# Kernel tuning notes

Hardware: AMD Instinct MI355X
Metric: run time of the kernel (lower is better)

## Reference

```python
import jax, jax.numpy as jnp
import numpy as np

B, S, H, HEADS = 4, 2048, 512, 8
DK = H // HEADS
LN_EPS = 1e-5
NEG_INF = -1e30


def setup_inputs() -> dict:
    key = jax.random.key(0)
    k = jax.random.split(key, 6)
    x = jax.random.normal(k[0], (B, S, H), dtype=jnp.float32)
    mask = jax.random.randint(k[1], (B, S), 0, 2, dtype=jnp.int32)
    # per-head Q/K/V projection weights stacked: [heads, H, dk]
    Wq = jax.random.normal(k[2], (HEADS, H, DK), dtype=jnp.float32) * 0.05
    Wk = jax.random.normal(k[3], (HEADS, H, DK), dtype=jnp.float32) * 0.05
    Wv = jax.random.normal(k[4], (HEADS, H, DK), dtype=jnp.float32) * 0.05
    # output projection: [heads*dk, H] (y = h @ Wo)
    Wo = jax.random.normal(k[5], (HEADS * DK, H), dtype=jnp.float32) * 0.05
    gamma = jnp.ones((H,), dtype=jnp.float32)
    beta = jnp.zeros((H,), dtype=jnp.float32)
    return {"x": x, "mask": mask, "Wq": Wq, "Wk": Wk, "Wv": Wv,
            "Wo": Wo, "gamma": gamma, "beta": beta}


def reference(x, mask, Wq, Wk, Wv, Wo, gamma, beta):
    # LayerNorm over hidden dim
    mu = jnp.mean(x, axis=-1, keepdims=True)
    var = jnp.mean(jnp.square(x - mu), axis=-1, keepdims=True)
    xn = (x - mu) * jax.lax.rsqrt(var + LN_EPS) * gamma + beta  # [B,S,H]

    mf = mask.astype(jnp.float32)  # [B,S]

    # batched per-head projections (original loops over heads)
    q = jnp.einsum('bsh,nhd->bnsd', xn, Wq)  # [B,heads,S,dk]
    kk = jnp.einsum('bsh,nhd->bnsd', xn, Wk)
    v = jnp.einsum('bsh,nhd->bnsd', xn, Wv)

    scores = jnp.einsum('bnqd,bnkd->bnqk', q, kk) / np.sqrt(DK).astype(np.float32)
    m = mf[:, None, None, :]  # [B,1,1,S] broadcast over query dim
    logits = m * scores + (1.0 - m) * NEG_INF
    probs = jax.nn.softmax(logits, axis=-1)
    attn = jnp.einsum('bnqk,bnkd->bnqd', probs, v)  # [B,heads,S,dk]

    h = attn.transpose(0, 2, 1, 3).reshape(x.shape[0], x.shape[1], HEADS * DK)
    out = h @ Wo + xn          # residual adds post-norm x (as in original)
    out = out * mf[:, :, None]  # zero out masked positions
    return out
```

## Files before the change

kernel.cpp:

```cpp
#include <hip/hip_runtime.h>
#include <hip/hip_bf16.h>
#include <math.h>

#define B_ 4
#define S_ 2048
#define H_ 512
#define HEADS_ 8
#define DK_ 64
#define NROWS_ (B_*S_)
#define LN_EPS_ 1e-5f
#define NEG_INF_ -1e30f
#define QSCALE_ (0.125f * 1.44269504088896f)

typedef short s8v __attribute__((ext_vector_type(8)));
typedef short s4v __attribute__((ext_vector_type(4)));
typedef float f4v __attribute__((ext_vector_type(4)));

typedef __attribute__((address_space(1))) unsigned int gu32_t;
typedef __attribute__((address_space(3))) unsigned int lu32_t;

__device__ __forceinline__ unsigned short f2bf(float f) {
    unsigned int u = __float_as_uint(f);
    u += 0x7FFFu + ((u >> 16) & 1u);
    return (unsigned short)(u >> 16);
}

__device__ __forceinline__ float bf2f(unsigned short u) {
    return __uint_as_float((unsigned int)u << 16);
}

__device__ __forceinline__ s4v pk4bf(float a, float b, float c, float d) {
    union { __hip_bfloat162 h[2]; s4v v; } u;
    u.h[0] = __float22bfloat162_rn(float2{a, b});
    u.h[1] = __float22bfloat162_rn(float2{c, d});
    return u.v;
}

__global__ __launch_bounds__(256) void prep_kernel(
        const float* __restrict__ x, const float* __restrict__ gamma,
        const float* __restrict__ beta, const int* __restrict__ mask,
        const float* __restrict__ Wq, const float* __restrict__ Wk,
        const float* __restrict__ Wv, const float* __restrict__ Wo,
        unsigned short* __restrict__ xnb, float* __restrict__ mb,
        unsigned short* __restrict__ Wt) {
    int bx = blockIdx.x;
    if (bx < 2048) {
        int row  = bx * 4 + (threadIdx.x >> 6);
        int lane = threadIdx.x & 63;
        const float4* xr = (const float4*)(x + (size_t)row * H_ + lane * 8);
        float4 a = xr[0], d = xr[1];
        float s  = (a.x + a.y) + (a.z + a.w) + (d.x + d.y) + (d.z + d.w);
        float ss = (a.x*a.x + a.y*a.y) + (a.z*a.z + a.w*a.w)
                 + (d.x*d.x + d.y*d.y) + (d.z*d.z + d.w*d.w);
        #pragma unroll
        for (int i = 1; i < 64; i <<= 1) {
            s  += __shfl_xor(s, i, 64);
            ss += __shfl_xor(ss, i, 64);
        }
        float mu  = s * (1.f / 512.f);
        float var = ss * (1.f / 512.f) - mu * mu;
        float rstd = rsqrtf(var + LN_EPS_);
        if (lane == 0) mb[row] = mask[row] ? 0.f : NEG_INF_;
        const float4* gp = (const float4*)(gamma + lane * 8);
        const float4* bp = (const float4*)(beta + lane * 8);
        float4 g0 = gp[0], g1 = gp[1], b0 = bp[0], b1 = bp[1];
        float4 y0, y1;
        y0.x = (a.x - mu) * rstd * g0.x + b0.x;
        y0.y = (a.y - mu) * rstd * g0.y + b0.y;
        y0.z = (a.z - mu) * rstd * g0.z + b0.z;
        y0.w = (a.w - mu) * rstd * g0.w + b0.w;
        y1.x = (d.x - mu) * rstd * g1.x + b1.x;
        y1.y = (d.y - mu) * rstd * g1.y + b1.y;
        y1.z = (d.z - mu) * rstd * g1.z + b1.z;
        y1.w = (d.w - mu) * rstd * g1.w + b1.w;
        union { s4v h[2]; s8v v; } pk;
        pk.h[0] = pk4bf(y0.x, y0.y, y0.z, y0.w);
        pk.h[1] = pk4bf(y1.x, y1.y, y1.z, y1.w);
        *(s8v*)(xnb + (size_t)row * H_ + lane * 8) = pk.v;
    } else {
        __shared__ float tile[32][33];
        int wid = bx - 2048;
        const float* src;
        int ld, drow, k0, c0;
        float scale = 1.f;
        if (wid < 768) {
            int z = wid >> 5, rem = wid & 31;
            int cx = rem & 1, ky = rem >> 1;
            k0 = ky * 32; c0 = cx * 32;
            int zw = z >> 3, head = z & 7;
            const float* W = (zw == 0) ? Wq : (zw == 1) ? Wk : Wv;
            if (zw == 0) scale = QSCALE_;
            src = W + (size_t)head * H_ * DK_;
            ld = DK_;
            drow = zw * 512 + head * 64;
        } else {
            int rem = wid - 768;
            int cx = rem & 15, ky = rem >> 4;
            k0 = ky * 32; c0 = cx * 32;
            src = Wo; ld = H_; drow = 1536;
        }
        int tx = threadIdx.x & 31, ty = threadIdx.x >> 5;
        #pragma unroll
        for (int i = 0; i < 4; i++)
            tile[ty * 4 + i][tx] = src[(size_t)(k0 + ty * 4 + i) * ld + c0 + tx];
        __syncthreads();
        #pragma unroll
        for (int i = 0; i < 4; i++) {
            int cc = ty * 4 + i;
            Wt[(size_t)(drow + c0 + cc) * 512 + k0 + tx] = f2bf(tile[tx][cc] * scale);
        }
    }
}

__device__ __forceinline__ void gemm_tile(
        const unsigned short* __restrict__ A,
        const unsigned short* __restrict__ Bt,
        int r0, int j0, f4v acc[4][4]) {
    __shared__ unsigned short As[2 * 128 * 32];
    __shared__ unsigned short Bs[2 * 128 * 32];
    int t = threadIdx.x;
    int wv = t >> 6, L = t & 63, c = L & 15, g = L >> 4;
    int m_base = (wv & 1) * 64, n_base = (wv >> 1) * 64;
    #pragma unroll
    for (int i = 0; i < 4; i++)
        #pragma unroll
        for (int j = 0; j < 4; j++) acc[i][j] = (f4v){0.f, 0.f, 0.f, 0.f};
    for (int k0 = 0; k0 < 512; k0 += 64) {
        __syncthreads();
        #pragma unroll
        for (int half = 0; half < 2; half++) {
            #pragma unroll
            for (int i = 0; i < 2; i++) {
                int u = wv * 128 + i * 64 + L;
                int row = u >> 2, k16 = u & 3;
                __builtin_amdgcn_global_load_lds(
                    (const gu32_t*)(A + (size_t)(r0 + row) * 512 + k0 + half * 32 + k16 * 8),
                    (lu32_t*)(As + half * 4096 + (size_t)(wv * 128 + i * 64) * 8), 16, 0, 0);
                __builtin_amdgcn_global_load_lds(
                    (const gu32_t*)(Bt + (size_t)(j0 + row) * 512 + k0 + half * 32 + k16 * 8),
                    (lu32_t*)(Bs + half * 4096 + (size_t)(wv * 128 + i * 64) * 8), 16, 0, 0);
            }
        }
        __asm__ volatile("s_waitcnt vmcnt(0)" ::: "memory");
        __syncthreads();
        #pragma unroll
        for (int half = 0; half < 2; half++) {
            s8v a[4], b[4];
            #pragma unroll
            for (int i = 0; i < 4; i++)
                a[i] = *(const s8v*)(As + half * 4096 + (size_t)(m_base + i * 16 + c) * 32 + g * 8);
            #pragma unroll
            for (int j = 0; j < 4; j++)
                b[j] = *(const s8v*)(Bs + half * 4096 + (size_t)(n_base + j * 16 + c) * 32 + g * 8);
            #pragma unroll
            for (int i = 0; i < 4; i++)
                #pragma unroll
                for (int j = 0; j < 4; j++)
                    acc[i][j] = __builtin_amdgcn_mfma_f32_16x16x32_bf16(
                        a[i], b[j], acc[i][j], 0, 0, 0);
        }
    }
}

__global__ __launch_bounds__(256) void qkv_gemm(
        const unsigned short* __restrict__ xnb,
        const unsigned short* __restrict__ Wt,
        unsigned short* __restrict__ Qb, unsigned short* __restrict__ Kf,
        unsigned short* __restrict__ Vf) {
    f4v acc[4][4];
    int t = threadIdx.x;
    int wv = t >> 6, L = t & 63, c = L & 15, g = L >> 4;
    int rb = wv & 1, cb = wv >> 1;
    if (blockIdx.x < 8) {
        int m0 = blockIdx.x * 128, n0 = blockIdx.y * 128;
        gemm_tile(Wt, xnb, m0, n0, acc);
        int R0 = m0 + rb * 64;
        int C0 = n0 + cb * 64;
        int hd = (R0 >> 6) & 7;
        int b  = C0 >> 11, srow0 = C0 & 2047;
        size_t bhbase = (size_t)(b * HEADS_ + hd) * S_ * DK_;
        if (R0 < 512) {
            #pragma unroll
            for (int msub = 0; msub < 4; msub++) {
                int dk4 = msub * 16 + g * 4;
                #pragma unroll
                for (int nsub = 0; nsub < 4; nsub++) {
                    int tok = srow0 + nsub * 16 + c;
                    s4v v = pk4bf(acc[msub][nsub][0], acc[msub][nsub][1],
                                  acc[msub][nsub][2], acc[msub][nsub][3]);
                    *(s4v*)(Qb + bhbase + (size_t)tok * DK_ + dk4) = v;
                }
            }
        } else {
            unsigned short* dst = Kf + bhbase + (size_t)(srow0 >> 6) * 4096;
            #pragma unroll
            for (int msub = 0; msub < 4; msub++) {
                int gx = (msub & 1) * 2 + (g >> 1);
                int slotbase = (g & 1) * 4 + (msub >> 1) * 8;
                #pragma unroll
                for (int nsub = 0; nsub < 4; nsub++) {
                    s4v v = pk4bf(acc[msub][nsub][0], acc[msub][nsub][1],
                                  acc[msub][nsub][2], acc[msub][nsub][3]);
                    *(s4v*)(dst + nsub * 1024 + (gx * 16 + c) * 16 + slotbase) = v;
                }
            }
        }
    } else {
        int r0 = blockIdx.y * 128, j0 = 1024 + (blockIdx.x - 8) * 128;
        gemm_tile(xnb, Wt, r0, j0, acc);
        int R0 = r0 + rb * 64;
        int C0 = j0 + cb * 64;
        int hd = (C0 >> 6) & 7;
        int b = R0 >> 11, srow0 = R0 & 2047;
        unsigned short* dst = Vf + (size_t)(b * HEADS_ + hd) * S_ * DK_
                              + (size_t)(srow0 >> 6) * 4096;
        #pragma unroll
        for (int msub = 0; msub < 4; msub++)
            #pragma unroll
            for (int nsub = 0; nsub < 4; nsub++) {
                s4v v = pk4bf(acc[msub][nsub][0], acc[msub][nsub][1],
                              acc[msub][nsub][2], acc[msub][nsub][3]);
                *(s4v*)(dst + nsub * 1024 + (g * 16 + c) * 16 + msub * 4) = v;
            }
    }
}

__global__ __launch_bounds__(256, 3) void attn_kernel(
        const unsigned short* __restrict__ Qb,
        const unsigned short* __restrict__ Kf,
        const unsigned short* __restrict__ Vf,
        const float* __restrict__ mb,
        unsigned short* __restrict__ hb) {
    __shared__ float red[2][64][2][17];

    int wv   = threadIdx.x >> 6;
    int qsub = wv & 1;
    int kp   = wv >> 1;
    int L  = threadIdx.x & 63;
    int c  = L & 15;
    int g  = L >> 4;
    int bh = blockIdx.y;
    int b  = bh >> 3, n = bh & 7;
    int q0 = blockIdx.x * 64 + qsub * 32;

    const unsigned short* Qbase = Qb + (size_t)bh * S_ * DK_;
    const unsigned short* Kp = Kf + (size_t)bh * S_ * DK_ + (size_t)kp * 16 * 4096 + L * 16;
    const unsigned short* Vp = Vf + (size_t)bh * S_ * DK_ + (size_t)kp * 16 * 4096 + L * 16;
    const float* mbrow = mb + b * S_ + kp * 1024;

    s8v qfA0 = *(const s8v*)(Qbase + (size_t)(q0 + c) * DK_ + g * 8);
    s8v qfA1 = *(const s8v*)(Qbase + (size_t)(q0 + c) * DK_ + 32 + g * 8);
    s8v qfB0 = *(const s8v*)(Qbase + (size_t)(q0 + 16 + c) * DK_ + g * 8);
    s8v qfB1 = *(const s8v*)(Qbase + (size_t)(q0 + 16 + c) * DK_ + 32 + g * 8);

    f4v accA[4], accB[4];
    #pragma unroll
    for (int i = 0; i < 4; i++) {
        accA[i] = (f4v){0.f, 0.f, 0.f, 0.f};
        accB[i] = (f4v){0.f, 0.f, 0.f, 0.f};
    }
    float lacA[4] = {0.f, 0.f, 0.f, 0.f};
    float lacB[4] = {0.f, 0.f, 0.f, 0.f};

    for (int kb = 0; kb < 16; kb++) {
        const unsigned short* Kn = Kp + (size_t)kb * 4096;
        const unsigned short* Vn = Vp + (size_t)kb * 4096;
        #pragma unroll
        for (int h = 0; h < 2; h++) {
            s8v k0lo = *(const s8v*)(Kn + (h * 2 + 0) * 1024);
            s8v k0hi = *(const s8v*)(Kn + (h * 2 + 0) * 1024 + 8);
            s8v k1lo = *(const s8v*)(Kn + (h * 2 + 1) * 1024);
            s8v k1hi = *(const s8v*)(Kn + (h * 2 + 1) * 1024 + 8);
            float4 mb0 = *(const float4*)(mbrow + kb * 64 + h * 32 + g * 4);
            float4 mb1 = *(const float4*)(mbrow + kb * 64 + h * 32 + 16 + g * 4);
            s8v vv[4];
            #pragma unroll
            for (int ds = 0; ds < 4; ds++)
                vv[ds] = *(const s8v*)(Vn + ds * 1024 + h * 8);
            f4v bias0 = (f4v){mb0.x, mb0.y, mb0.z, mb0.w};
            f4v bias1 = (f4v){mb1.x, mb1.y, mb1.z, mb1.w};
            f4v sA0 = bias0, sA1 = bias1, sB0 = bias0, sB1 = bias1;
            sA0 = __builtin_amdgcn_mfma_f32_16x16x32_bf16(k0lo, qfA0, sA0, 0, 0, 0);
            sA0 = __builtin_amdgcn_mfma_f32_16x16x32_bf16(k0hi, qfA1, sA0, 0, 0, 0);
            sA1 = __builtin_amdgcn_mfma_f32_16x16x32_bf16(k1lo, qfA0, sA1, 0, 0, 0);
            sA1 = __builtin_amdgcn_mfma_f32_16x16x32_bf16(k1hi, qfA1, sA1, 0, 0, 0);
            sB0 = __builtin_amdgcn_mfma_f32_16x16x32_bf16(k0lo, qfB0, sB0, 0, 0, 0);
            sB0 = __builtin_amdgcn_mfma_f32_16x16x32_bf16(k0hi, qfB1, sB0, 0, 0, 0);
            sB1 = __builtin_amdgcn_mfma_f32_16x16x32_bf16(k1lo, qfB0, sB1, 0, 0, 0);
            sB1 = __builtin_amdgcn_mfma_f32_16x16x32_bf16(k1hi, qfB1, sB1, 0, 0, 0);
            float pA0[4], pA1[4], pB0[4], pB1[4];
            #pragma unroll
            for (int r = 0; r < 4; r++) {
                pA0[r] = __builtin_amdgcn_exp2f(sA0[r]);
                pA1[r] = __builtin_amdgcn_exp2f(sA1[r]);
                pB0[r] = __builtin_amdgcn_exp2f(sB0[r]);
                pB1[r] = __builtin_amdgcn_exp2f(sB1[r]);
                lacA[r] += pA0[r] + pA1[r];
                lacB[r] += pB0[r] + pB1[r];
            }
            s4v pfA0 = pk4bf(pA0[0], pA0[1], pA0[2], pA0[3]);
            s4v pfA1 = pk4bf(pA1[0], pA1[1], pA1[2], pA1[3]);
            s4v pfB0 = pk4bf(pB0[0], pB0[1], pB0[2], pB0[3]);
            s4v pfB1 = pk4bf(pB1[0], pB1[1], pB1[2], pB1[3]);
            #pragma unroll
            for (int ds = 0; ds < 4; ds++) {
                s4v v0 = __builtin_shufflevector(vv[ds], vv[ds], 0, 1, 2, 3);
                s4v v1 = __builtin_shufflevector(vv[ds], vv[ds], 4, 5, 6, 7);
                accA[ds] = __builtin_amdgcn_mfma_f32_16x16x16bf16_1k(v0, pfA0, accA[ds], 0, 0, 0);
                accA[ds] = __builtin_amdgcn_mfma_f32_16x16x16bf16_1k(v1, pfA1, accA[ds], 0, 0, 0);
                accB[ds] = __builtin_amdgcn_mfma_f32_16x16x16bf16_1k(v0, pfB0, accB[ds], 0, 0, 0);
                accB[ds] = __builtin_amdgcn_mfma_f32_16x16x16bf16_1k(v1, pfB1, accB[ds], 0, 0, 0);
            }
        }
    }

    float lA = (lacA[0] + lacA[1]) + (lacA[2] + lacA[3]);
    float lB = (lacB[0] + lacB[1]) + (lacB[2] + lacB[3]);
    lA += __shfl_xor(lA, 16, 64);
    lA += __shfl_xor(lA, 32, 64);
    lB += __shfl_xor(lB, 16, 64);
    lB += __shfl_xor(lB, 32, 64);

    if (kp == 1) {
        #pragma unroll
        for (int d = 0; d < 4; d++) {
            #pragma unroll
            for (int r = 0; r < 4; r++) {
                red[qsub][L][0][d * 4 + r] = accA[d][r];
                red[qsub][L][1][d * 4 + r] = accB[d][r];
            }
        }
        red[qsub][L][0][16] = lA;
        red[qsub][L][1][16] = lB;
    }
    __syncthreads();
    if (kp == 0) {
        const float* srcA = &red[qsub][L][0][0];
        const float* srcB = &red[qsub][L][1][0];
        float invA = 1.f / (lA + srcA[16]);
        float invB = 1.f / (lB + srcB[16]);
        unsigned short* hpA = hb + (size_t)(b * S_ + q0 + c) * H_ + n * DK_ + g * 4;
        unsigned short* hpB = hpA + (size_t)16 * H_;
        #pragma unroll
        for (int ds = 0; ds < 4; ds++) {
            s4v oA = pk4bf((accA[ds][0] + srcA[ds * 4 + 0]) * invA,
                           (accA[ds][1] + srcA[ds * 4 + 1]) * invA,
                           (accA[ds][2] + srcA[ds * 4 + 2]) * invA,
                           (accA[ds][3] + srcA[ds * 4 + 3]) * invA);
            *(s4v*)(hpA + ds * 16) = oA;
            s4v oB = pk4bf((accB[ds][0] + srcB[ds * 4 + 0]) * invB,
                           (accB[ds][1] + srcB[ds * 4 + 1]) * invB,
                           (accB[ds][2] + srcB[ds * 4 + 2]) * invB,
                           (accB[ds][3] + srcB[ds * 4 + 3]) * invB);
            *(s4v*)(hpB + ds * 16) = oB;
        }
    }
}

__global__ __launch_bounds__(256) void out_gemm(
        const unsigned short* __restrict__ hb,
        const unsigned short* __restrict__ Wot,
        const unsigned short* __restrict__ xnb, const int* __restrict__ mask,
        float* __restrict__ out) {
    f4v acc[4][4];
    int r0 = blockIdx.y * 128, j0 = blockIdx.x * 128;
    gemm_tile(hb, Wot, r0, j0, acc);
    int t = threadIdx.x;
    int wv = t >> 6, L = t & 63, c = L & 15, g = L >> 4;
    int mrow = r0 + (wv & 1) * 64 + g * 4;
    int ncol = j0 + (wv >> 1) * 64 + c;
    #pragma unroll
    for (int msub = 0; msub < 4; msub++) {
        #pragma unroll
        for (int rr = 0; rr < 4; rr++) {
            int row = mrow + msub * 16 + rr;
            float mf = (float)mask[row];
            #pragma unroll
            for (int nsub = 0; nsub < 4; nsub++) {
                int col = ncol + nsub * 16;
                size_t o = (size_t)row * H_ + col;
                out[o] = (acc[msub][nsub][rr] + bf2f(xnb[o])) * mf;
            }
        }
    }
}

extern "C" void kernel_launch(void* const* d_in, const int* in_sizes, int n_in,
                              void* d_out, int out_size, void* d_ws, size_t ws_size,
                              hipStream_t stream) {
    const float* x     = (const float*)d_in[0];
    const int*   mask  = (const int*)d_in[1];
    const float* Wq    = (const float*)d_in[2];
    const float* Wk    = (const float*)d_in[3];
    const float* Wv    = (const float*)d_in[4];
    const float* Wo    = (const float*)d_in[5];
    const float* gamma = (const float*)d_in[6];
    const float* beta  = (const float*)d_in[7];
    float* out = (float*)d_out;

    size_t nelem = (size_t)NROWS_ * H_;
    char* ws = (char*)d_ws;
    unsigned short* xnb = (unsigned short*)ws; ws += nelem * 2;
    unsigned short* hb  = (unsigned short*)ws; ws += nelem * 2;
    unsigned short* Qb  = (unsigned short*)ws; ws += nelem * 2;
    unsigned short* Kf  = (unsigned short*)ws; ws += nelem * 2;
    unsigned short* Vf  = (unsigned short*)ws; ws += nelem * 2;
    unsigned short* Wt  = (unsigned short*)ws; ws += (size_t)2048 * 512 * 2;
    float*          mbp = (float*)ws;

    prep_kernel<<<3072, 256, 0, stream>>>(
        x, gamma, beta, mask, Wq, Wk, Wv, Wo, xnb, mbp, Wt);
    qkv_gemm<<<dim3(12, 64), 256, 0, stream>>>(xnb, Wt, Qb, Kf, Vf);
    attn_kernel<<<dim3(S_ / 64, B_ * HEADS_), 256, 0, stream>>>(
        Qb, Kf, Vf, mbp, hb);
    out_gemm<<<dim3(4, 64), 256, 0, stream>>>(
        hb, Wt + (size_t)1536 * 512, xnb, mask, out);
}
```

Before: 179.2 us.

## Drop split-K attention; each wave covers all keys for its own queries

The attention kernel previously split the key range across two wave pairs and merged partial accumulators and row sums through shared memory with a block barrier. Now each of the four waves owns 32 distinct queries and loops over all 32 key blocks, so a block covers 128 queries and the grid is halved. This removes the LDS reduction and __syncthreads and doubles reuse of each K/V tile across four query groups per block. In exchange each wave runs a serial loop twice as long and there are half as many blocks (512), which may lower latency hiding and occupancy balance across CUs.

Result: slower. 200.3 us (+11.8%).

```diff
diff --git a/kernel.cpp b/kernel.cpp
--- a/kernel.cpp
+++ b/kernel.cpp
@@ -231,22 +231,18 @@
         const unsigned short* __restrict__ Vf,
         const float* __restrict__ mb,
         unsigned short* __restrict__ hb) {
-    __shared__ float red[2][64][2][17];
-
-    int wv   = threadIdx.x >> 6;
-    int qsub = wv & 1;
-    int kp   = wv >> 1;
+    int wv = threadIdx.x >> 6;
     int L  = threadIdx.x & 63;
     int c  = L & 15;
     int g  = L >> 4;
     int bh = blockIdx.y;
     int b  = bh >> 3, n = bh & 7;
-    int q0 = blockIdx.x * 64 + qsub * 32;
+    int q0 = blockIdx.x * 128 + wv * 32;
 
     const unsigned short* Qbase = Qb + (size_t)bh * S_ * DK_;
-    const unsigned short* Kp = Kf + (size_t)bh * S_ * DK_ + (size_t)kp * 16 * 4096 + L * 16;
-    const unsigned short* Vp = Vf + (size_t)bh * S_ * DK_ + (size_t)kp * 16 * 4096 + L * 16;
-    const float* mbrow = mb + b * S_ + kp * 1024;
+    const unsigned short* Kp = Kf + (size_t)bh * S_ * DK_ + L * 16;
+    const unsigned short* Vp = Vf + (size_t)bh * S_ * DK_ + L * 16;
+    const float* mbrow = mb + b * S_;
 
     s8v qfA0 = *(const s8v*)(Qbase + (size_t)(q0 + c) * DK_ + g * 8);
     s8v qfA1 = *(const s8v*)(Qbase + (size_t)(q0 + c) * DK_ + 32 + g * 8);
@@ -262,7 +258,7 @@
     float lacA[4] = {0.f, 0.f, 0.f, 0.f};
     float lacB[4] = {0.f, 0.f, 0.f, 0.f};
 
-    for (int kb = 0; kb < 16; kb++) {
+    for (int kb = 0; kb < 32; kb++) {
         const unsigned short* Kn = Kp + (size_t)kb * 4096;
         const unsigned short* Vn = Vp + (size_t)kb * 4096;
         #pragma unroll
@@ -320,40 +316,19 @@
     lA += __shfl_xor(lA, 32, 64);
     lB += __shfl_xor(lB, 16, 64);
     lB += __shfl_xor(lB, 32, 64);
-
-    if (kp == 1) {
-        #pragma unroll
-        for (int d = 0; d < 4; d++) {
-            #pragma unroll
-            for (int r = 0; r < 4; r++) {
-                red[qsub][L][0][d * 4 + r] = accA[d][r];
-                red[qsub][L][1][d * 4 + r] = accB[d][r];
-            }
-        }
-        red[qsub][L][0][16] = lA;
-        red[qsub][L][1][16] = lB;
-    }
-    __syncthreads();
-    if (kp == 0) {
-        const float* srcA = &red[qsub][L][0][0];
-        const float* srcB = &red[qsub][L][1][0];
-        float invA = 1.f / (lA + srcA[16]);
-        float invB = 1.f / (lB + srcB[16]);
-        unsigned short* hpA = hb + (size_t)(b * S_ + q0 + c) * H_ + n * DK_ + g * 4;
-        unsigned short* hpB = hpA + (size_t)16 * H_;
-        #pragma unroll
-        for (int ds = 0; ds < 4; ds++) {
-            s4v oA = pk4bf((accA[ds][0] + srcA[ds * 4 + 0]) * invA,
-                           (accA[ds][1] + srcA[ds * 4 + 1]) * invA,
-                           (accA[ds][2] + srcA[ds * 4 + 2]) * invA,
-                           (accA[ds][3] + srcA[ds * 4 + 3]) * invA);
-            *(s4v*)(hpA + ds * 16) = oA;
-            s4v oB = pk4bf((accB[ds][0] + srcB[ds * 4 + 0]) * invB,
-                           (accB[ds][1] + srcB[ds * 4 + 1]) * invB,
-                           (accB[ds][2] + srcB[ds * 4 + 2]) * invB,
-                           (accB[ds][3] + srcB[ds * 4 + 3]) * invB);
-            *(s4v*)(hpB + ds * 16) = oB;
-        }
+    float invA = 1.f / lA;
+    float invB = 1.f / lB;
+
+    unsigned short* hpA = hb + (size_t)(b * S_ + q0 + c) * H_ + n * DK_ + g * 4;
+    unsigned short* hpB = hpA + (size_t)16 * H_;
+    #pragma unroll
+    for (int ds = 0; ds < 4; ds++) {
+        s4v oA = pk4bf(accA[ds][0] * invA, accA[ds][1] * invA,
+                       accA[ds][2] * invA, accA[ds][3] * invA);
+        *(s4v*)(hpA + ds * 16) = oA;
+        s4v oB = pk4bf(accB[ds][0] * invB, accB[ds][1] * invB,
+                       accB[ds][2] * invB, accB[ds][3] * invB);
+        *(s4v*)(hpB + ds * 16) = oB;
     }
 }
 
@@ -411,7 +386,7 @@
     prep_kernel<<<3072, 256, 0, stream>>>(
         x, gamma, beta, mask, Wq, Wk, Wv, Wo, xnb, mbp, Wt);
     qkv_gemm<<<dim3(12, 64), 256, 0, stream>>>(xnb, Wt, Qb, Kf, Vf);
-    attn_kernel<<<dim3(S_ / 64, B_ * HEADS_), 256, 0, stream>>>(
+    attn_kernel<<<dim3(S_ / 128, B_ * HEADS_), 256, 0, stream>>>(
         Qb, Kf, Vf, mbp, hb);
     out_gemm<<<dim3(4, 64), 256, 0, stream>>>(
         hb, Wt + (size_t)1536 * 512, xnb, mask, out);
```
